# Kernel tuning notes

Measured on AMD Instinct MI355X. Metric: run time of the kernel, lower is better.

Reference implementation:

```python
import jax, jax.numpy as jnp
import numpy as np

B, N, NVT, HS, NZ = 512, 256, 32, 128, 64


def setup_inputs() -> dict:
    key = jax.random.key(0)
    ks = jax.random.split(key, 16)
    node_types = jax.random.randint(ks[0], (B, N), 0, NVT, dtype=jnp.int32)
    node_types = node_types.at[:, 0].set(0)      # START_TYPE
    node_types = node_types.at[:, -1].set(1)     # END_TYPE
    adj = jax.random.randint(ks[1], (B, N, N), 0, 2, dtype=jnp.int32)
    # DAG: edges only u -> v with u < v (strict upper triangular)
    tri = jnp.triu(jnp.ones((N, N), jnp.int32), k=1)
    adj = adj * tri[None, :, :]
    s = 0.05
    p = lambda k, shp: (jax.random.normal(k, shp, jnp.float32) * s)
    return {
        "node_types": node_types,
        "adj": adj,
        "W_ih": p(ks[2], (3 * HS, NVT)),   # grue_forward weight_ih
        "W_hh": p(ks[3], (3 * HS, HS)),    # grue_forward weight_hh
        "b_ih": p(ks[4], (3 * HS,)),
        "b_hh": p(ks[5], (3 * HS,)),
        "Wg": p(ks[6], (HS, NVT)),         # gate_forward linear
        "bg": p(ks[7], (HS,)),
        "Wm": p(ks[8], (HS, NVT)),         # mapper_forward (no bias)
        "W1": p(ks[9], (NZ, HS)),          # fc1 -> mu
        "b1": p(ks[10], (NZ,)),
        "W2": p(ks[11], (NZ, HS)),         # fc2 -> logvar
        "b2": p(ks[12], (NZ,)),
    }


def reference(node_types, adj, W_ih, W_hh, b_ih, b_hh, Wg, bg, Wm, W1, b1, W2, b2):
    hs = Wg.shape[0]
    # one-hot vertex types  [B, N, nvt]
    X = jax.nn.one_hot(node_types, Wg.shape[1], dtype=W_ih.dtype)
    # gated message from each vertex's TYPE (mapper has no bias -> padding contributes 0)
    gated = jax.nn.sigmoid(jnp.einsum('bnv,hv->bnh', X, Wg) + bg) \
            * jnp.einsum('bnv,hv->bnh', X, Wm)                      # [B, N, hs]
    A = adj.astype(gated.dtype)
    # predecessor aggregation: H_v = sum_{u: u->v} gated_u
    Hpre = jnp.einsum('buv,buh->bvh', A, gated)                     # [B, N, hs]
    # torch GRUCell(X_v, Hpre_v), vectorized over all vertices (no recurrence:
    # messages depend only on predecessor types)
    gi = jnp.einsum('bnv,gv->bng', X, W_ih) + b_ih                  # [B, N, 3hs]
    gh = jnp.einsum('bnh,gh->bng', Hpre, W_hh) + b_hh
    r = jax.nn.sigmoid(gi[..., :hs] + gh[..., :hs])
    z = jax.nn.sigmoid(gi[..., hs:2 * hs] + gh[..., hs:2 * hs])
    n = jnp.tanh(gi[..., 2 * hs:] + r * gh[..., 2 * hs:])
    Hv = (1.0 - z) * n + z * Hpre                                   # H_forward, [B, N, hs]
    # graph state: sum over vertices [1, N-1) (start=1, end_offset=1)
    Hg = Hv[:, 1:-1, :].sum(axis=1)                                 # [B, hs]
    mu = Hg @ W1.T + b1
    logvar = Hg @ W2.T + b2
    return (mu, logvar)
```

## Files before the change

### kernel.cpp

```cpp
#include <hip/hip_runtime.h>
#include <hip/hip_bf16.h>

#define HS 128
#define NVT 32
#define NN 256

typedef __attribute__((ext_vector_type(8))) short bf16x8;
typedef __attribute__((ext_vector_type(4))) short s16x4;
typedef __attribute__((ext_vector_type(4))) float f32x4;
typedef __attribute__((ext_vector_type(4))) unsigned uint4v;
typedef unsigned long long u64;

#define TABB_OFF 0
#define GIT_OFF  32768
#define RBG_OFF  65536

static __device__ __forceinline__ short f2bs(float f) {
    __hip_bfloat16 h = __float2bfloat16(f);
    short s; __builtin_memcpy(&s, &h, 2);
    return s;
}
static __device__ __forceinline__ float bs2f(short s) {
    __hip_bfloat16 h; __builtin_memcpy(&h, &s, 2);
    return __bfloat162float(h);
}
static __device__ __forceinline__ float sigm(float x) {
    return __builtin_amdgcn_rcpf(1.f + __expf(-x));
}
static __device__ __forceinline__ u64 shflx64(u64 x, int m) {
    unsigned lo = (unsigned)x, hi = (unsigned)(x >> 32);
    lo = (unsigned)__shfl_xor((int)lo, m);
    hi = (unsigned)__shfl_xor((int)hi, m);
    return ((u64)hi << 32) | lo;
}

__global__ void __launch_bounds__(512) build_tables(
    const float* __restrict__ W_ih, const float* __restrict__ W_hh,
    const float* __restrict__ b_ih, const float* __restrict__ b_hh,
    const float* __restrict__ Wg,   const float* __restrict__ bg,
    const float* __restrict__ Wm,
    short* __restrict__ TABB, short* __restrict__ GIT)
{
    __shared__ float G_s[HS];
    const int t = blockIdx.x;
    const int j = threadIdx.x;
    if (j < HS) {
        float x = Wg[j * NVT + t] + bg[j];
        G_s[j] = sigm(x) * Wm[j * NVT + t];
    }
    __syncthreads();
    if (j < 384) {
        float acc = 0.f;
        for (int h = 0; h < HS; ++h) acc += G_s[h] * W_hh[j * HS + h];
        TABB[j * NVT + t] = f2bs(acc);
        float git = W_ih[j * NVT + t] + b_ih[j];
        if (j < 256) git += b_hh[j];
        GIT[t * 512 + (j & 127) * 4 + (j >> 7)] = f2bs(git);
    } else {
        TABB[j * NVT + t] = f2bs(G_s[j - 384]);
    }
}

__global__ void __launch_bounds__(256) dvae_bitpack(
    const int* __restrict__ adj, u64* __restrict__ rbg)
{
    const int lane = threadIdx.x & 63;
    const int wid = blockIdx.x * 4 + (threadIdx.x >> 6);
    const uint4v* ap = (const uint4v*)adj;
    #pragma unroll
    for (int it = 0; it < 2; ++it) {
        const int r0 = wid + it * 65536;
        uint4v a[4];
        #pragma unroll
        for (int k = 0; k < 4; ++k)
            a[k] = __builtin_nontemporal_load(&ap[(size_t)(r0 + k * 16384) * 64 + lane]);
        #pragma unroll
        for (int k = 0; k < 4; ++k) {
            const int r = r0 + k * 16384;
            u64 b0 = __ballot(a[k].x != 0u), b1 = __ballot(a[k].y != 0u);
            u64 b2 = __ballot(a[k].z != 0u), b3 = __ballot(a[k].w != 0u);
            u64 v = (lane & 2) ? ((lane & 1) ? b3 : b2) : ((lane & 1) ? b1 : b0);
            if (lane < 4)
                rbg[((r >> 8) << 10) + (lane << 8) + (r & 255)] = v;
        }
    }
}

__global__ void __launch_bounds__(512) dvae_gru2(
    const int* __restrict__ node_types, const u64* __restrict__ rbg,
    const short* __restrict__ TABB, const short* __restrict__ GIT,
    const float* __restrict__ b_hh,
    const float* __restrict__ W1, const float* __restrict__ b1,
    const float* __restrict__ W2, const float* __restrict__ b2,
    float* __restrict__ out)
{
    __shared__ u64 RBs[4 * 256];
    __shared__ u64 Ct[4 * 256];
    __shared__ u64 Tm[NVT * 4];
    __shared__ unsigned cntA[256 * 20];
    __shared__ int types_s[NN];
    __shared__ float hg_s[HS];

    const int b = blockIdx.x, tid = threadIdx.x;
    const int wave = tid >> 6, lane = tid & 63;
    const int quad = lane >> 4, col = lane & 15;

    if (tid < NN) types_s[tid] = node_types[b * NN + tid];
    RBs[tid]       = rbg[(size_t)b * 1024 + tid];
    RBs[tid + 512] = rbg[(size_t)b * 1024 + 512 + tid];

    bf16x8 bfrag[4];
    #pragma unroll
    for (int g = 0; g < 4; ++g) {
        int jb = (g < 3 ? g * 128 : 384) + wave * 16;
        bfrag[g] = *(const bf16x8*)(TABB + (jb + col) * 32 + quad * 8);
    }
    const int h0 = wave * 16 + col;
    const float bhn = b_hh[256 + h0];
    __syncthreads();

    if (wave < 4) {
        int ty = types_s[wave * 64 + lane];
        u64 myb = 0;
        #pragma unroll
        for (int t = 0; t < NVT; ++t) {
            u64 bb = __ballot(ty == t);
            if (lane == t) myb = bb;
        }
        if (lane < NVT) Tm[lane * 4 + wave] = myb;
    }

    constexpr u64 TMS[6] = {
        0x5555555555555555ULL, 0x3333333333333333ULL, 0x0F0F0F0F0F0F0F0FULL,
        0x00FF00FF00FF00FFULL, 0x0000FFFF0000FFFFULL, 0x00000000FFFFFFFFULL };
    #pragma unroll
    for (int k2 = 0; k2 < 2; ++k2) {
        int id = wave * 2 + k2, i = id >> 2, j = id & 3;
        u64 x = RBs[j * 256 + i * 64 + lane];
        #pragma unroll
        for (int s = 5; s >= 0; --s) {
            int jj = 1 << s;
            u64 m = TMS[s];
            u64 y = shflx64(x, jj);
            x = (lane & jj) ? ((x & ~m) | ((y >> jj) & m))
                            : ((x & m) | ((y & m) << jj));
        }
        Ct[i * 256 + j * 64 + lane] = x;
    }
    __syncthreads();

    {
        const int cp = tid & 255, tg = tid >> 8;
        u64 cc0 = Ct[cp], cc1 = Ct[256 + cp], cc2 = Ct[512 + cp], cc3 = Ct[768 + cp];
        unsigned ow[8];
        #pragma unroll
        for (int k = 0; k < 8; ++k) {
            int tp = tg * 8 + k;
            const u64* T0 = &Tm[(2 * tp) * 4];
            const u64* T1 = &Tm[(2 * tp + 1) * 4];
            unsigned c0 = __popcll(cc0 & T0[0]) + __popcll(cc1 & T0[1])
                        + __popcll(cc2 & T0[2]) + __popcll(cc3 & T0[3]);
            unsigned c1 = __popcll(cc0 & T1[0]) + __popcll(cc1 & T1[1])
                        + __popcll(cc2 & T1[2]) + __popcll(cc3 & T1[3]);
            ow[k] = (__float_as_uint((float)c0) >> 16)
                  | (__float_as_uint((float)c1) & 0xFFFF0000u);
        }
        *(uint4*)&cntA[cp * 20 + tg * 8]     = *(const uint4*)&ow[0];
        *(uint4*)&cntA[cp * 20 + tg * 8 + 4] = *(const uint4*)&ow[4];
    }
    __syncthreads();

    float hg = 0.f;
    for (int m = 0; m < 16; ++m) {
        bf16x8 afrag = *(const bf16x8*)(cntA + (m * 16 + col) * 20 + quad * 4);
        f32x4 acc[4];
        #pragma unroll
        for (int g = 0; g < 4; ++g)
            acc[g] = __builtin_amdgcn_mfma_f32_16x16x32_bf16(
                afrag, bfrag[g], (f32x4){0.f, 0.f, 0.f, 0.f}, 0, 0, 0);
        #pragma unroll
        for (int r = 0; r < 4; ++r) {
            int cpr = m * 16 + quad * 4 + r;
            int vv = ((cpr & 63) << 2) | (cpr >> 6);
            int tv = types_s[vv];
            s16x4 gv = *(const s16x4*)(GIT + tv * 512 + h0 * 4);
            float gir = bs2f(gv[0]);
            float giz = bs2f(gv[1]);
            float gin = bs2f(gv[2]);
            float rr = sigm(gir + acc[0][r]);
            float zz = sigm(giz + acc[1][r]);
            float x2 = gin + rr * (acc[2][r] + bhn);
            float nt = 1.f - 2.f * __builtin_amdgcn_rcpf(1.f + __expf(2.f * x2));
            float msk = (vv >= 1 && vv < NN - 1) ? 1.f : 0.f;
            hg += msk * ((1.f - zz) * nt + zz * acc[3][r]);
        }
    }
    hg += __shfl_xor(hg, 16);
    hg += __shfl_xor(hg, 32);
    if (lane < 16) hg_s[h0] = hg;
    __syncthreads();

    if (tid < 128) {
        int which = tid >> 6, zz = tid & 63;
        const float* W = which ? W2 : W1;
        float acc2 = which ? b2[zz] : b1[zz];
        const float4* Wv = (const float4*)(W + zz * HS);
        #pragma unroll
        for (int i = 0; i < 32; ++i) {
            float4 ww = Wv[i];
            acc2 += hg_s[4 * i] * ww.x + hg_s[4 * i + 1] * ww.y
                  + hg_s[4 * i + 2] * ww.z + hg_s[4 * i + 3] * ww.w;
        }
        out[which * 32768 + b * 64 + zz] = acc2;
    }
}

extern "C" void kernel_launch(void* const* d_in, const int* in_sizes, int n_in,
                              void* d_out, int out_size, void* d_ws, size_t ws_size,
                              hipStream_t stream)
{
    const int* node_types = (const int*)d_in[0];
    const int* adj        = (const int*)d_in[1];
    const float* W_ih = (const float*)d_in[2];
    const float* W_hh = (const float*)d_in[3];
    const float* b_ih = (const float*)d_in[4];
    const float* b_hh = (const float*)d_in[5];
    const float* Wg   = (const float*)d_in[6];
    const float* bg   = (const float*)d_in[7];
    const float* Wm   = (const float*)d_in[8];
    const float* W1   = (const float*)d_in[9];
    const float* b1   = (const float*)d_in[10];
    const float* W2   = (const float*)d_in[11];
    const float* b2   = (const float*)d_in[12];

    char* ws = (char*)d_ws;
    short* TABB = (short*)(ws + TABB_OFF);
    short* GIT  = (short*)(ws + GIT_OFF);
    u64*   RBG  = (u64*)(ws + RBG_OFF);
    float* out  = (float*)d_out;

    dvae_bitpack<<<dim3(4096), dim3(256), 0, stream>>>(adj, RBG);
    build_tables<<<dim3(32), dim3(512), 0, stream>>>(W_ih, W_hh, b_ih, b_hh, Wg, bg, Wm, TABB, GIT);
    dvae_gru2<<<dim3(512), dim3(512), 0, stream>>>(node_types, RBG, TABB, GIT, b_hh, W1, b1, W2, b2, out);
}
```

Before: 249.5 us.

## Fuse adjacency bit-packing into the GRU kernel, dropping the separate pass

Removes the standalone bitpack kernel and its global workspace buffer. Each GRU block now loads its own batch's adjacency rows and ballot-packs them straight into shared memory. This avoids a launch and the round trip of the packed bitmask through global memory. In exchange, the large adjacency read is now issued by fewer, heavier blocks and may get lower memory-level parallelism than the wide dedicated kernel had.

```diff
diff --git a/kernel.cpp b/kernel.cpp
--- a/kernel.cpp
+++ b/kernel.cpp
@@ -13,7 +13,6 @@
 
 #define TABB_OFF 0
 #define GIT_OFF  32768
-#define RBG_OFF  65536
 
 static __device__ __forceinline__ short f2bs(float f) {
     __hip_bfloat16 h = __float2bfloat16(f);
@@ -61,33 +60,8 @@
     }
 }
 
-__global__ void __launch_bounds__(256) dvae_bitpack(
-    const int* __restrict__ adj, u64* __restrict__ rbg)
-{
-    const int lane = threadIdx.x & 63;
-    const int wid = blockIdx.x * 4 + (threadIdx.x >> 6);
-    const uint4v* ap = (const uint4v*)adj;
-    #pragma unroll
-    for (int it = 0; it < 2; ++it) {
-        const int r0 = wid + it * 65536;
-        uint4v a[4];
-        #pragma unroll
-        for (int k = 0; k < 4; ++k)
-            a[k] = __builtin_nontemporal_load(&ap[(size_t)(r0 + k * 16384) * 64 + lane]);
-        #pragma unroll
-        for (int k = 0; k < 4; ++k) {
-            const int r = r0 + k * 16384;
-            u64 b0 = __ballot(a[k].x != 0u), b1 = __ballot(a[k].y != 0u);
-            u64 b2 = __ballot(a[k].z != 0u), b3 = __ballot(a[k].w != 0u);
-            u64 v = (lane & 2) ? ((lane & 1) ? b3 : b2) : ((lane & 1) ? b1 : b0);
-            if (lane < 4)
-                rbg[((r >> 8) << 10) + (lane << 8) + (r & 255)] = v;
-        }
-    }
-}
-
-__global__ void __launch_bounds__(512) dvae_gru2(
-    const int* __restrict__ node_types, const u64* __restrict__ rbg,
+__global__ void __launch_bounds__(512) dvae_fused2(
+    const int* __restrict__ node_types, const int* __restrict__ adj,
     const short* __restrict__ TABB, const short* __restrict__ GIT,
     const float* __restrict__ b_hh,
     const float* __restrict__ W1, const float* __restrict__ b1,
@@ -106,8 +80,26 @@
     const int quad = lane >> 4, col = lane & 15;
 
     if (tid < NN) types_s[tid] = node_types[b * NN + tid];
-    RBs[tid]       = rbg[(size_t)b * 1024 + tid];
-    RBs[tid + 512] = rbg[(size_t)b * 1024 + 512 + tid];
+
+    {
+        const uint4v* ap = (const uint4v*)(adj + (size_t)b * NN * NN);
+        #pragma unroll
+        for (int k = 0; k < 4; ++k) {
+            const int u0 = wave * 32 + k * 8;
+            uint4v a[8];
+            #pragma unroll
+            for (int j = 0; j < 8; ++j)
+                a[j] = ap[(size_t)(u0 + j) * 64 + lane];
+            #pragma unroll
+            for (int j = 0; j < 8; ++j) {
+                u64 b0 = __ballot(a[j].x != 0u), b1 = __ballot(a[j].y != 0u);
+                u64 b2 = __ballot(a[j].z != 0u), b3 = __ballot(a[j].w != 0u);
+                u64 v = (lane & 2) ? ((lane & 1) ? b3 : b2) : ((lane & 1) ? b1 : b0);
+                if (lane < 4)
+                    RBs[(lane << 8) + u0 + j] = v;
+            }
+        }
+    }
 
     bf16x8 bfrag[4];
     #pragma unroll
@@ -236,10 +228,8 @@
     char* ws = (char*)d_ws;
     short* TABB = (short*)(ws + TABB_OFF);
     short* GIT  = (short*)(ws + GIT_OFF);
-    u64*   RBG  = (u64*)(ws + RBG_OFF);
     float* out  = (float*)d_out;
 
-    dvae_bitpack<<<dim3(4096), dim3(256), 0, stream>>>(adj, RBG);
     build_tables<<<dim3(32), dim3(512), 0, stream>>>(W_ih, W_hh, b_ih, b_hh, Wg, bg, Wm, TABB, GIT);
-    dvae_gru2<<<dim3(512), dim3(512), 0, stream>>>(node_types, RBG, TABB, GIT, b_hh, W1, b1, W2, b2, out);
-}
+    dvae_fused2<<<dim3(512), dim3(512), 0, stream>>>(node_types, adj, TABB, GIT, b_hh, W1, b1, W2, b2, out);
+}
```

Result: faster. 242.0 us (-3.0%).
